# Kernel tuning notes

Measured on AMD Instinct MI355X. Metric: run time of the kernel, lower is better.

Reference implementation:

```python
import jax, jax.numpy as jnp
import numpy as np

FRAME_LEN = 1024
HOP_LEN = 256
T_WAV = 8388608
N_FRAMES = (T_WAV - FRAME_LEN) // HOP_LEN + 1  # 32765


def setup_inputs() -> dict:
    key = jax.random.key(0)
    k1, k2, k3, k4 = jax.random.split(key, 4)
    wav = 0.1 * jax.random.normal(k1, (T_WAV,), dtype=jnp.float32)
    # realistic F0 range [80, 400) Hz
    src_f0 = 80.0 + 320.0 * jax.random.uniform(k2, (N_FRAMES,), dtype=jnp.float32)
    tgt_f0 = 80.0 + 320.0 * jax.random.uniform(k3, (N_FRAMES,), dtype=jnp.float32)
    voiced_mask = jax.random.uniform(k4, (N_FRAMES,)) < 0.8
    return {"wav": wav, "src_f0": src_f0, "tgt_f0": tgt_f0, "voiced_mask": voiced_mask}


def _psola(wav, src_f0, tgt_f0, voiced_mask):
    L, hop = FRAME_LEN, HOP_LEN
    T = wav.shape[0]
    nf = min(src_f0.shape[0], (T - L) // hop + 1)  # frames that fully fit (loop breaks otherwise)
    starts = jnp.arange(nf, dtype=jnp.int32) * hop
    idx = starts[:, None] + jnp.arange(L, dtype=jnp.int32)[None, :]  # [nf, L]
    frames = wav[idx]  # [nf, L]

    src = src_f0[:nf]
    tgt = tgt_f0[:nf]
    # frames with src_f0<1 or tgt_f0<1 pass through unchanged, as do unvoiced frames
    valid = voiced_mask[:nf] & (src >= 1.0) & (tgt >= 1.0)
    ratio = jnp.clip(src / jnp.where(tgt >= 1.0, tgt, 1.0), 0.25, 4.0)
    # round-half-to-even matches Python round()
    new_len = jnp.maximum(1, jnp.round(L * ratio)).astype(jnp.int32)  # [nf]

    # F.interpolate(mode='linear', align_corners=False): x = (j+0.5)*L/new_len - 0.5
    scale = jnp.float32(L) / new_len.astype(jnp.float32)  # [nf]
    j = jnp.arange(L, dtype=jnp.float32)
    x = jnp.clip((j[None, :] + 0.5) * scale[:, None] - 0.5, 0.0, L - 1)  # [nf, L]
    x0 = jnp.floor(x).astype(jnp.int32)
    x1 = jnp.minimum(x0 + 1, L - 1)
    w = x - x0.astype(jnp.float32)
    rows = jnp.arange(nf, dtype=jnp.int32)[:, None]
    resamp = frames[rows, x0] * (1.0 - w) + frames[rows, x1] * w  # [nf, L]
    # if new_len < L, output is zero-padded past new_len; if >= L, take first L
    resamp = jnp.where(j[None, :] < new_len[:, None].astype(jnp.float32), resamp, 0.0)

    shifted = jnp.where(valid[:, None], resamp, frames)

    # Hann-windowed overlap-add (torch.hann_window is periodic)
    hann = 0.5 - 0.5 * jnp.cos(2.0 * jnp.pi * jnp.arange(L, dtype=jnp.float32) / L)
    out = jnp.zeros((T,), dtype=wav.dtype).at[idx].add(shifted * hann[None, :])
    weights = jnp.zeros((T,), dtype=wav.dtype).at[idx].add(
        jnp.broadcast_to(hann[None, :], (nf, L)))
    return jnp.where(weights > 1e-8, out / jnp.where(weights > 1e-8, weights, 1.0), out)


def reference(wav, src_f0, tgt_f0, voiced_mask):
    return _psola(wav, src_f0, tgt_f0, voiced_mask)
```

## Files before the change

### kernel.cpp

```cpp
#include <hip/hip_runtime.h>
#include <math.h>

#define T_WAV    8388608
#define FRAME_L  1024
#define HOP      256
#define NF       32765
#define NBLK4    (T_WAV / 1024)

__device__ __forceinline__ bool detect_byte_layout(const unsigned int* mask_words,
                                                   int tid) {
    __shared__ int s_flag;
    if (tid == 0) s_flag = 0;
    __syncthreads();
    unsigned w = mask_words[tid & 255];
    if ((w & 0xFFFFFF00u) != 0u && w != 0xFFFFFFFFu) atomicOr(&s_flag, 1);
    __syncthreads();
    return s_flag != 0;
}

__global__ __launch_bounds__(256) void psola_prepass(
    const float* __restrict__ src_f0,
    const float* __restrict__ tgt_f0,
    const unsigned int* __restrict__ mask_words,
    float* __restrict__ scale_t,
    int*   __restrict__ enc_t)
{
    bool bytelay = detect_byte_layout(mask_words, threadIdx.x);
    int f = blockIdx.x * 256 + threadIdx.x;
    if (f < NF) {
        float src = src_f0[f];
        float tgt = tgt_f0[f];
        const unsigned char* m8 = (const unsigned char*)mask_words;
        unsigned off = bytelay ? (unsigned)f : ((unsigned)f << 2);
        bool valid = (m8[off] != 0) && (src >= 1.0f) && (tgt >= 1.0f);
        float denom = (tgt >= 1.0f) ? tgt : 1.0f;
        float ratio = fminf(fmaxf(src / denom, 0.25f), 4.0f);
        int nl = (int)rintf(1024.0f * ratio);
        if (nl < 1) nl = 1;
        scale_t[f] = 1024.0f / (float)nl;
        enc_t[f]   = valid ? nl : -1;
    }
}

__global__ __launch_bounds__(256) void psola_main4(
    const float* __restrict__ wav,
    const float* __restrict__ scale_t,
    const int*   __restrict__ enc_t,
    float*       __restrict__ out)
{
    __shared__ float s_wav[2564];

    const int p   = blockIdx.x;
    const int L   = ((p & 7) << 10) + (p >> 3);
    const int tid = threadIdx.x;
    const int B   = L << 10;

    const int b0 = L << 2;
    const int f0 = (b0 > 3) ? (b0 - 3) : 0;
    const int f1 = ((b0 + 3) < NF - 1) ? (b0 + 3) : (NF - 1);
    const int base = f0 << 8;
    const int wlen = ((f1 - f0) << 8) + 1024;

    {
        const float4* g4 = (const float4*)(wav + base);
        float4*       s4 = (float4*)s_wav;
        const int nv = wlen >> 2;
        for (int i = tid; i < nv; i += 256) s4[i] = g4[i];
    }
    if (tid == 0) s_wav[wlen] = 0.0f;

    int   enc[7];
    float scl[7];
    #pragma unroll
    for (int i = 0; i < 7; ++i) {
        int f = f0 + i;
        if (f <= f1) { enc[i] = enc_t[f]; scl[i] = scale_t[f]; }
        else         { enc[i] = -1;       scl[i] = 1.0f; }
    }

    float hh[4], jf[4];
    #pragma unroll
    for (int m = 0; m < 4; ++m) {
        int j = tid + (m << 8);
        hh[m] = 0.5f - 0.5f * cospif((float)j * (1.0f / 512.0f));
        jf[m] = (float)j + 0.5f;
    }
    float wsum4 = hh[0] + hh[1] + hh[2] + hh[3];
    float rw4   = (wsum4 > 1e-8f) ? (1.0f / wsum4) : 1.0f;

    __syncthreads();

    if (f0 == b0 - 3 && b0 + 3 <= NF - 1) {
        #pragma unroll
        for (int k = 0; k < 4; ++k) {
            const int loc_t = (k << 8) + tid + 768;
            float acc = 0.0f;
            #pragma unroll
            for (int q = 0; q < 4; ++q) {
                const int   fi = k + q;
                const int   e  = enc[fi];
                const int   m  = 3 - q;
                float val;
                if (e < 0) {
                    val = s_wav[loc_t];
                } else if ((tid + (m << 8)) < e) {
                    float s  = scl[fi];
                    float x  = fminf(fmaxf(fmaf(jf[m], s, -0.5f), 0.0f), 1023.0f);
                    int   x0 = (int)x;
                    float w2 = x - (float)x0;
                    const float* pp = &s_wav[(fi << 8) + x0];
                    float v0 = pp[0];
                    float v1 = pp[1];
                    val = fmaf(w2, v1 - v0, v0);
                } else {
                    val = 0.0f;
                }
                acc = fmaf(val, hh[m], acc);
            }
            out[B + (k << 8) + tid] = acc * rw4;
        }
    } else {
        for (int k = 0; k < 4; ++k) {
            const int t  = B + (k << 8) + tid;
            const int bt = t >> 8;
            int lo = bt - 3; if (lo < 0) lo = 0;
            int hi = bt;     if (hi > NF - 1) hi = NF - 1;
            float acc = 0.0f, wsum = 0.0f;
            for (int f = lo; f <= hi; ++f) {
                const int fi = f - f0;
                const int j  = t - (f << 8);
                const int m  = j >> 8;
                const float h = hh[m];
                const int   e = enc[fi];
                float val;
                if (e < 0) {
                    val = s_wav[t - base];
                } else if (j < e) {
                    float s  = scl[fi];
                    float x  = fminf(fmaxf(fmaf(jf[m], s, -0.5f), 0.0f), 1023.0f);
                    int   x0 = (int)x;
                    float w2 = x - (float)x0;
                    const float* pp = &s_wav[(fi << 8) + x0];
                    float v0 = pp[0];
                    float v1 = pp[1];
                    val = fmaf(w2, v1 - v0, v0);
                } else {
                    val = 0.0f;
                }
                acc  = fmaf(val, h, acc);
                wsum += h;
            }
            out[t] = (wsum > 1e-8f) ? (acc / wsum) : acc;
        }
    }
}

__global__ __launch_bounds__(256) void psola_fallback(
    const float* __restrict__ wav,
    const float* __restrict__ src_f0,
    const float* __restrict__ tgt_f0,
    const unsigned int* __restrict__ mask_words,
    float*       __restrict__ out)
{
    bool bytelay = detect_byte_layout(mask_words, threadIdx.x);
    const unsigned char* m8 = (const unsigned char*)mask_words;

    int t = blockIdx.x * 256 + threadIdx.x;
    int a    = t - (FRAME_L - 1);
    int f_lo = (a > 0) ? ((a + HOP - 1) >> 8) : 0;
    int f_hi = t >> 8;
    if (f_hi > NF - 1) f_hi = NF - 1;

    float wt = wav[t], acc = 0.0f, wsum = 0.0f;
    for (int f = f_lo; f <= f_hi; ++f) {
        int   j = t - (f << 8);
        float h = 0.5f - 0.5f * cospif((float)j * (1.0f / 512.0f));
        float src = src_f0[f], tgt = tgt_f0[f];
        unsigned off = bytelay ? (unsigned)f : ((unsigned)f << 2);
        bool valid = (m8[off] != 0) && (src >= 1.0f) && (tgt >= 1.0f);
        float val;
        if (valid) {
            float denom = (tgt >= 1.0f) ? tgt : 1.0f;
            float ratio = fminf(fmaxf(src / denom, 0.25f), 4.0f);
            int nl = (int)rintf(1024.0f * ratio);
            if (nl < 1) nl = 1;
            if (j < nl) {
                float s  = 1024.0f / (float)nl;
                float x  = fminf(fmaxf(((float)j + 0.5f) * s - 0.5f, 0.0f), 1023.0f);
                int   x0 = (int)floorf(x);
                int   x1 = x0 + 1; if (x1 > 1023) x1 = 1023;
                float w2 = x - (float)x0;
                const float* fr = wav + (f << 8);
                val = fr[x0] * (1.0f - w2) + fr[x1] * w2;
            } else val = 0.0f;
        } else val = wt;
        acc += val * h; wsum += h;
    }
    out[t] = (wsum > 1e-8f) ? (acc / wsum) : acc;
}

extern "C" void kernel_launch(void* const* d_in, const int* in_sizes, int n_in,
                              void* d_out, int out_size, void* d_ws, size_t ws_size,
                              hipStream_t stream) {
    const float*        wav  = (const float*)d_in[0];
    const float*        src  = (const float*)d_in[1];
    const float*        tgt  = (const float*)d_in[2];
    const unsigned int* mask = (const unsigned int*)d_in[3];
    float*              out  = (float*)d_out;

    const size_t need = (32768 + 32768) * 4;
    if (ws_size >= need) {
        float* scale_t = (float*)d_ws;
        int*   enc_t   = (int*)(scale_t + 32768);
        psola_prepass<<<128, 256, 0, stream>>>(src, tgt, mask, scale_t, enc_t);
        psola_main4<<<NBLK4, 256, 0, stream>>>(wav, scale_t, enc_t, out);
    } else {
        psola_fallback<<<T_WAV / 256, 256, 0, stream>>>(wav, src, tgt, mask, out);
    }
}
```

Measured before the change: 99.53 us.

## Fuse per-frame prepass into main kernel with larger 2048-sample blocks

Removes the separate prepass kernel and its workspace round-trip. Each block now computes its own frame ratios and lengths into shared memory. Blocks grow to 512 threads covering 2048 output samples, which shrinks the halo overhead of the shared wav tile, and outputs are written with nontemporal stores. The mask layout detection is redone per thread from 16 words, and the fallback path that ran without a workspace is dropped. The larger shared-memory footprint may reduce occupancy.

```diff
diff --git a/kernel.cpp b/kernel.cpp
--- a/kernel.cpp
+++ b/kernel.cpp
@@ -1,33 +1,55 @@
 #include <hip/hip_runtime.h>
 #include <math.h>
 
-#define T_WAV    8388608
-#define FRAME_L  1024
-#define HOP      256
-#define NF       32765
-#define NBLK4    (T_WAV / 1024)
+#define T_WAV   8388608
+#define FRAME_L 1024
+#define HOP     256
+#define NF      32765
+#define OUT_PB  2048
+#define NBLK    (T_WAV / OUT_PB)
+#define NTHR    512
 
-__device__ __forceinline__ bool detect_byte_layout(const unsigned int* mask_words,
-                                                   int tid) {
-    __shared__ int s_flag;
-    if (tid == 0) s_flag = 0;
-    __syncthreads();
-    unsigned w = mask_words[tid & 255];
-    if ((w & 0xFFFFFF00u) != 0u && w != 0xFFFFFFFFu) atomicOr(&s_flag, 1);
-    __syncthreads();
-    return s_flag != 0;
-}
-
-__global__ __launch_bounds__(256) void psola_prepass(
+__global__ __launch_bounds__(512) void psola_fused(
+    const float* __restrict__ wav,
     const float* __restrict__ src_f0,
     const float* __restrict__ tgt_f0,
     const unsigned int* __restrict__ mask_words,
-    float* __restrict__ scale_t,
-    int*   __restrict__ enc_t)
+    float*       __restrict__ out)
 {
-    bool bytelay = detect_byte_layout(mask_words, threadIdx.x);
-    int f = blockIdx.x * 256 + threadIdx.x;
-    if (f < NF) {
+    __shared__ float s_wav[3588];
+    __shared__ float s_scl[11];
+    __shared__ int   s_enc[11];
+
+    const int p   = blockIdx.x;
+    const int L   = ((p & 7) << 9) + (p >> 3);
+    const int tid = threadIdx.x;
+    const int tl  = tid & 255;
+    const int th  = tid >> 8;
+
+    const int b0   = L << 3;
+    const int B    = L << 11;
+    const int f0   = (b0 > 3) ? (b0 - 3) : 0;
+    const int f1   = ((b0 + 7) < NF - 1) ? (b0 + 7) : (NF - 1);
+    const int base = f0 << 8;
+    const int wlen = ((f1 - f0) << 8) + 1024;
+
+    {
+        const float4* g4 = (const float4*)(wav + base);
+        float4*       s4 = (float4*)s_wav;
+        const int nv = wlen >> 2;
+        for (int i = tid; i < nv; i += NTHR) s4[i] = g4[i];
+    }
+    if (tid == 0) s_wav[wlen] = 0.0f;
+
+    const int nfr = f1 - f0 + 1;
+    if (tid < nfr) {
+        bool bytelay = false;
+        #pragma unroll
+        for (int i = 0; i < 16; ++i) {
+            unsigned w = mask_words[i];
+            if ((w & 0xFFFFFF00u) != 0u && w != 0xFFFFFFFFu) bytelay = true;
+        }
+        const int f = f0 + tid;
         float src = src_f0[f];
         float tgt = tgt_f0[f];
         const unsigned char* m8 = (const unsigned char*)mask_words;
@@ -37,51 +59,14 @@
         float ratio = fminf(fmaxf(src / denom, 0.25f), 4.0f);
         int nl = (int)rintf(1024.0f * ratio);
         if (nl < 1) nl = 1;
-        scale_t[f] = 1024.0f / (float)nl;
-        enc_t[f]   = valid ? nl : -1;
-    }
-}
-
-__global__ __launch_bounds__(256) void psola_main4(
-    const float* __restrict__ wav,
-    const float* __restrict__ scale_t,
-    const int*   __restrict__ enc_t,
-    float*       __restrict__ out)
-{
-    __shared__ float s_wav[2564];
-
-    const int p   = blockIdx.x;
-    const int L   = ((p & 7) << 10) + (p >> 3);
-    const int tid = threadIdx.x;
-    const int B   = L << 10;
-
-    const int b0 = L << 2;
-    const int f0 = (b0 > 3) ? (b0 - 3) : 0;
-    const int f1 = ((b0 + 3) < NF - 1) ? (b0 + 3) : (NF - 1);
-    const int base = f0 << 8;
-    const int wlen = ((f1 - f0) << 8) + 1024;
-
-    {
-        const float4* g4 = (const float4*)(wav + base);
-        float4*       s4 = (float4*)s_wav;
-        const int nv = wlen >> 2;
-        for (int i = tid; i < nv; i += 256) s4[i] = g4[i];
-    }
-    if (tid == 0) s_wav[wlen] = 0.0f;
-
-    int   enc[7];
-    float scl[7];
-    #pragma unroll
-    for (int i = 0; i < 7; ++i) {
-        int f = f0 + i;
-        if (f <= f1) { enc[i] = enc_t[f]; scl[i] = scale_t[f]; }
-        else         { enc[i] = -1;       scl[i] = 1.0f; }
+        s_scl[tid] = 1024.0f / (float)nl;
+        s_enc[tid] = valid ? nl : -1;
     }
 
     float hh[4], jf[4];
     #pragma unroll
     for (int m = 0; m < 4; ++m) {
-        int j = tid + (m << 8);
+        int j = tl + (m << 8);
         hh[m] = 0.5f - 0.5f * cospif((float)j * (1.0f / 512.0f));
         jf[m] = (float)j + 0.5f;
     }
@@ -90,21 +75,22 @@
 
     __syncthreads();
 
-    if (f0 == b0 - 3 && b0 + 3 <= NF - 1) {
+    if (f0 == b0 - 3 && (b0 + 7) <= NF - 1) {
         #pragma unroll
         for (int k = 0; k < 4; ++k) {
-            const int loc_t = (k << 8) + tid + 768;
+            const int c     = (k << 1) + th;
+            const int loc_t = (c << 8) + tl + 768;
             float acc = 0.0f;
             #pragma unroll
             for (int q = 0; q < 4; ++q) {
-                const int   fi = k + q;
-                const int   e  = enc[fi];
-                const int   m  = 3 - q;
+                const int fi = c + q;
+                const int m  = 3 - q;
+                const int e  = s_enc[fi];
                 float val;
                 if (e < 0) {
                     val = s_wav[loc_t];
-                } else if ((tid + (m << 8)) < e) {
-                    float s  = scl[fi];
+                } else if ((tl + (m << 8)) < e) {
+                    float s  = s_scl[fi];
                     float x  = fminf(fmaxf(fmaf(jf[m], s, -0.5f), 0.0f), 1023.0f);
                     int   x0 = (int)x;
                     float w2 = x - (float)x0;
@@ -117,11 +103,11 @@
                 }
                 acc = fmaf(val, hh[m], acc);
             }
-            out[B + (k << 8) + tid] = acc * rw4;
+            __builtin_nontemporal_store(acc * rw4, &out[B + (k << 9) + tid]);
         }
     } else {
         for (int k = 0; k < 4; ++k) {
-            const int t  = B + (k << 8) + tid;
+            const int t  = B + (k << 9) + tid;
             const int bt = t >> 8;
             int lo = bt - 3; if (lo < 0) lo = 0;
             int hi = bt;     if (hi > NF - 1) hi = NF - 1;
@@ -131,12 +117,12 @@
                 const int j  = t - (f << 8);
                 const int m  = j >> 8;
                 const float h = hh[m];
-                const int   e = enc[fi];
+                const int   e = s_enc[fi];
                 float val;
                 if (e < 0) {
                     val = s_wav[t - base];
                 } else if (j < e) {
-                    float s  = scl[fi];
+                    float s  = s_scl[fi];
                     float x  = fminf(fmaxf(fmaf(jf[m], s, -0.5f), 0.0f), 1023.0f);
                     int   x0 = (int)x;
                     float w2 = x - (float)x0;
@@ -150,53 +136,10 @@
                 acc  = fmaf(val, h, acc);
                 wsum += h;
             }
-            out[t] = (wsum > 1e-8f) ? (acc / wsum) : acc;
+            float o = (wsum > 1e-8f) ? (acc / wsum) : acc;
+            __builtin_nontemporal_store(o, &out[t]);
         }
     }
-}
-
-__global__ __launch_bounds__(256) void psola_fallback(
-    const float* __restrict__ wav,
-    const float* __restrict__ src_f0,
-    const float* __restrict__ tgt_f0,
-    const unsigned int* __restrict__ mask_words,
-    float*       __restrict__ out)
-{
-    bool bytelay = detect_byte_layout(mask_words, threadIdx.x);
-    const unsigned char* m8 = (const unsigned char*)mask_words;
-
-    int t = blockIdx.x * 256 + threadIdx.x;
-    int a    = t - (FRAME_L - 1);
-    int f_lo = (a > 0) ? ((a + HOP - 1) >> 8) : 0;
-    int f_hi = t >> 8;
-    if (f_hi > NF - 1) f_hi = NF - 1;
-
-    float wt = wav[t], acc = 0.0f, wsum = 0.0f;
-    for (int f = f_lo; f <= f_hi; ++f) {
-        int   j = t - (f << 8);
-        float h = 0.5f - 0.5f * cospif((float)j * (1.0f / 512.0f));
-        float src = src_f0[f], tgt = tgt_f0[f];
-        unsigned off = bytelay ? (unsigned)f : ((unsigned)f << 2);
-        bool valid = (m8[off] != 0) && (src >= 1.0f) && (tgt >= 1.0f);
-        float val;
-        if (valid) {
-            float denom = (tgt >= 1.0f) ? tgt : 1.0f;
-            float ratio = fminf(fmaxf(src / denom, 0.25f), 4.0f);
-            int nl = (int)rintf(1024.0f * ratio);
-            if (nl < 1) nl = 1;
-            if (j < nl) {
-                float s  = 1024.0f / (float)nl;
-                float x  = fminf(fmaxf(((float)j + 0.5f) * s - 0.5f, 0.0f), 1023.0f);
-                int   x0 = (int)floorf(x);
-                int   x1 = x0 + 1; if (x1 > 1023) x1 = 1023;
-                float w2 = x - (float)x0;
-                const float* fr = wav + (f << 8);
-                val = fr[x0] * (1.0f - w2) + fr[x1] * w2;
-            } else val = 0.0f;
-        } else val = wt;
-        acc += val * h; wsum += h;
-    }
-    out[t] = (wsum > 1e-8f) ? (acc / wsum) : acc;
 }
 
 extern "C" void kernel_launch(void* const* d_in, const int* in_sizes, int n_in,
@@ -208,13 +151,5 @@
     const unsigned int* mask = (const unsigned int*)d_in[3];
     float*              out  = (float*)d_out;
 
-    const size_t need = (32768 + 32768) * 4;
-    if (ws_size >= need) {
-        float* scale_t = (float*)d_ws;
-        int*   enc_t   = (int*)(scale_t + 32768);
-        psola_prepass<<<128, 256, 0, stream>>>(src, tgt, mask, scale_t, enc_t);
-        psola_main4<<<NBLK4, 256, 0, stream>>>(wav, scale_t, enc_t, out);
-    } else {
-        psola_fallback<<<T_WAV / 256, 256, 0, stream>>>(wav, src, tgt, mask, out);
-    }
+    psola_fused<<<NBLK, NTHR, 0, stream>>>(wav, src, tgt, mask, out);
 }
```

New measurement: 100.3 us. About the same (+0.8%).
